# Kernel optimization log

Hardware: AMD Instinct MI355X
Metric: run time of the kernel (lower is better)

Reference implementation:

```python
import jax, jax.numpy as jnp
import numpy as np

B, H, S, D = 8, 16, 1024, 128

def setup_inputs() -> dict:
    key = jax.random.key(0)
    kq, kk, kv = jax.random.split(key, 3)
    q = jax.random.normal(kq, (B, H, S, D), dtype=jnp.float32)
    k = jax.random.normal(kk, (B, H, S, D), dtype=jnp.float32)
    v = jax.random.normal(kv, (B, H, S, D), dtype=jnp.float32)
    return {"q": q, "k": k, "v": v}

def reference(q, k, v):
    dims = q.shape[-1]
    # scores[..., j, i] = sum_k q[..., j, k] * k_[..., i, k]; note scale is 1/dims (not 1/sqrt(dims))
    scores = jnp.einsum('bhjd,bhid->bhji', q, k) / dims
    probs = jax.nn.softmax(scores, axis=-1)
    out = jnp.einsum('bhji,bhid->bhjd', probs, v)
    return out
```

## Files before the change

kernel.cpp:

```cpp
#include <hip/hip_runtime.h>

#define S_LEN 1024
#define D_DIM 128
#define KVBLK 32
#define BH_N 128

typedef __attribute__((ext_vector_type(8))) short short8;
typedef __attribute__((ext_vector_type(4))) short short4v;
typedef __attribute__((ext_vector_type(4))) float f32x4;
typedef __attribute__((ext_vector_type(16))) float f32x16;
typedef __attribute__((ext_vector_type(4))) unsigned int uint4v;

__device__ __forceinline__ unsigned short f2bf(float f) {
  union { float f; unsigned u; } x; x.f = f;
  unsigned r = x.u + 0x7fffu + ((x.u >> 16) & 1u);
  return (unsigned short)(r >> 16);
}

__device__ __forceinline__ short8 pack8(float4 a, float4 b) {
  short8 f;
  f[0] = (short)f2bf(a.x); f[1] = (short)f2bf(a.y);
  f[2] = (short)f2bf(a.z); f[3] = (short)f2bf(a.w);
  f[4] = (short)f2bf(b.x); f[5] = (short)f2bf(b.y);
  f[6] = (short)f2bf(b.z); f[7] = (short)f2bf(b.w);
  return f;
}

__device__ __forceinline__ void gload_lds16(const void* g, void* l) {
  __builtin_amdgcn_global_load_lds(
      (const __attribute__((address_space(1))) unsigned int*)g,
      (__attribute__((address_space(3))) unsigned int*)l, 16, 0, 0);
}

__global__ __launch_bounds__(256) void conv_k(const float* __restrict__ in,
                                              unsigned short* __restrict__ out,
                                              int n8) {
  int i = blockIdx.x * 256 + threadIdx.x;
  int stride = gridDim.x * 256;
  for (; i < n8; i += stride) {
    float4 a = ((const float4*)in)[i * 2];
    float4 b = ((const float4*)in)[i * 2 + 1];
    ((short8*)out)[i] = pack8(a, b);
  }
}

__global__ __launch_bounds__(256) void conv_vt(const float* __restrict__ v,
                                               unsigned short* __restrict__ vt) {
  __shared__ unsigned short tile[64][72];
  int b = blockIdx.x;
  int d0 = (b & 1) * 64;
  int s0 = ((b >> 1) & 15) * 64;
  int bh = b >> 5;
  int t = threadIdx.x;
  #pragma unroll
  for (int i = 0; i < 4; ++i) {
    int s = (t >> 4) + i * 16;
    int dl = (t & 15) * 4;
    float4 x = *(const float4*)(v + ((size_t)(bh * S_LEN) + s0 + s) * D_DIM + d0 + dl);
    tile[s][dl + 0] = f2bf(x.x); tile[s][dl + 1] = f2bf(x.y);
    tile[s][dl + 2] = f2bf(x.z); tile[s][dl + 3] = f2bf(x.w);
  }
  __syncthreads();
  #pragma unroll
  for (int i = 0; i < 2; ++i) {
    int j = i * 256 + t;
    int dl = j >> 3, sc = j & 7;
    short8 w;
    #pragma unroll
    for (int q = 0; q < 8; ++q) w[q] = (short)tile[sc * 8 + q][dl];
    *(short8*)(vt + ((size_t)(bh * D_DIM) + d0 + dl) * S_LEN + s0 + sc * 8) = w;
  }
}

__global__ __launch_bounds__(256, 4) void attn_main(
    const float* __restrict__ qg, const unsigned short* __restrict__ kbf,
    const unsigned short* __restrict__ vtbf, float* __restrict__ og) {
  __shared__ unsigned short K_lds[2][KVBLK * D_DIM];
  __shared__ unsigned short VT_lds[2][D_DIM * KVBLK];

  const int tid = threadIdx.x;
  const int lane = tid & 63;
  const int wid = tid >> 6;
  const int l31 = lane & 31;
  const int hi = lane >> 5;

  const int bid = blockIdx.x;
  const int bh = (bid & 7) | ((bid >> 6) << 3);
  const int qt = (bid >> 3) & 7;

  const size_t base = (size_t)bh * (S_LEN * D_DIM);
  const int qw = qt * 128 + wid * 32;

  short8 qf[8];
  {
    const float* qp = qg + base + (size_t)(qw + l31) * D_DIM + hi * 8;
    const float s = 0.0078125f * 1.44269504088896f;
    #pragma unroll
    for (int c = 0; c < 8; ++c) {
      float4 a = *(const float4*)(qp + c * 16);
      float4 b = *(const float4*)(qp + c * 16 + 4);
      a.x *= s; a.y *= s; a.z *= s; a.w *= s;
      b.x *= s; b.y *= s; b.z *= s; b.w *= s;
      qf[c] = pack8(a, b);
    }
  }

  float l_r = 0.f;
  f32x16 o_acc[4];
  #pragma unroll
  for (int dt = 0; dt < 4; ++dt)
    #pragma unroll
    for (int r = 0; r < 16; ++r) o_acc[dt][r] = 0.f;

  const char* kbB = (const char*)(kbf + base);
  const char* vtB = (const char*)(vtbf + (size_t)bh * (D_DIM * S_LEN));

  int koffA, koffB, voff;
  {
    int r0 = wid * 8 + (lane >> 4);
    int c = lane & 15;
    koffA = (r0 * D_DIM + ((c ^ (r0 & 7)) * 8)) * 2;
    int r1 = r0 + 4;
    koffB = (r1 * D_DIM + ((c ^ (r1 & 7)) * 8)) * 2;
    int d0 = wid * 32 + (lane >> 2);
    int c2 = lane & 3;
    voff = (d0 * S_LEN + ((c2 ^ (lane >> 4)) * 8)) * 2;
  }
  const int KRB = l31 * 256 + ((hi ^ (l31 & 7)) << 4);
  const int VRB = l31 * 64 + ((hi ^ ((l31 >> 2) & 3)) << 4);

  #define STAGE(buf, tnext)                                                    \
    {                                                                          \
      const char* ks = kbB + (tnext) * (KVBLK * D_DIM * 2);                    \
      gload_lds16(ks + koffA, &K_lds[buf][(wid * 8) * D_DIM]);                 \
      gload_lds16(ks + koffB, &K_lds[buf][(wid * 8 + 4) * D_DIM]);             \
      const char* vs = vtB + (tnext) * (KVBLK * 2);                            \
      gload_lds16(vs + voff, &VT_lds[buf][(wid * 32) * KVBLK]);                \
      gload_lds16(vs + voff + 16 * S_LEN * 2,                                  \
                  &VT_lds[buf][(wid * 32 + 16) * KVBLK]);                      \
    }

  STAGE(0, 0);
  __syncthreads();

  for (int t = 0; t < S_LEN / KVBLK; ++t) {
    const int cur = t & 1;
    if (t + 1 < S_LEN / KVBLK) STAGE(cur ^ 1, t + 1);

    const char* kl = (const char*)&K_lds[cur][0];
    const char* vl = (const char*)&VT_lds[cur][0];

    f32x16 sacc;
    #pragma unroll
    for (int r = 0; r < 16; ++r) sacc[r] = 0.f;

    __builtin_amdgcn_s_setprio(1);
    #pragma unroll
    for (int c = 0; c < 8; ++c) {
      short8 kf = *(const short8*)(kl + (KRB ^ (c << 5)));
      sacc = __builtin_amdgcn_mfma_f32_32x32x16_bf16(kf, qf[c], sacc, 0, 0, 0);
    }
    __builtin_amdgcn_s_setprio(0);

    #pragma unroll
    for (int c = 0; c < 2; ++c) {
      float p0 = exp2f(fminf(sacc[8 * c + 0], 80.f));
      float p1 = exp2f(fminf(sacc[8 * c + 1], 80.f));
      unsigned w0;
      asm("v_cvt_pk_bf16_f32 %0, %1, %2" : "=v"(w0) : "v"(p0), "v"(p1));
      float p2 = exp2f(fminf(sacc[8 * c + 2], 80.f));
      float p3 = exp2f(fminf(sacc[8 * c + 3], 80.f));
      unsigned w1;
      asm("v_cvt_pk_bf16_f32 %0, %1, %2" : "=v"(w1) : "v"(p2), "v"(p3));
      l_r += (p0 + p1) + (p2 + p3);
      float p4 = exp2f(fminf(sacc[8 * c + 4], 80.f));
      float p5 = exp2f(fminf(sacc[8 * c + 5], 80.f));
      unsigned w2;
      asm("v_cvt_pk_bf16_f32 %0, %1, %2" : "=v"(w2) : "v"(p4), "v"(p5));
      float p6 = exp2f(fminf(sacc[8 * c + 6], 80.f));
      float p7 = exp2f(fminf(sacc[8 * c + 7], 80.f));
      unsigned w3;
      asm("v_cvt_pk_bf16_f32 %0, %1, %2" : "=v"(w3) : "v"(p6), "v"(p7));
      l_r += (p4 + p5) + (p6 + p7);

      asm volatile("v_permlane32_swap_b32 %0, %1" : "+v"(w0), "+v"(w2));
      asm volatile("v_permlane32_swap_b32 %0, %1" : "+v"(w1), "+v"(w3));
      uint4v pw;
      pw[0] = w0; pw[1] = w1; pw[2] = w2; pw[3] = w3;
      short8 pa = __builtin_bit_cast(short8, pw);

      __builtin_amdgcn_s_setprio(1);
      const int vx = VRB ^ (c << 5);
      #pragma unroll
      for (int dt = 0; dt < 4; ++dt) {
        short8 vf = *(const short8*)(vl + vx + dt * 2048);
        o_acc[dt] = __builtin_amdgcn_mfma_f32_32x32x16_bf16(pa, vf, o_acc[dt], 0, 0, 0);
      }
      __builtin_amdgcn_s_setprio(0);
    }
    __syncthreads();
  }

  float lsum = l_r + __shfl_xor(l_r, 32);
  float linv = 1.0f / lsum;
  #pragma unroll
  for (int r = 0; r < 16; ++r) {
    int qr = (r & 3) + 8 * (r >> 2) + 4 * hi;
    float lv = __shfl(linv, qr, 64);
    #pragma unroll
    for (int dt = 0; dt < 4; ++dt) {
      og[base + (size_t)(qw + qr) * D_DIM + dt * 32 + l31] = o_acc[dt][r] * lv;
    }
  }
}

__global__ __launch_bounds__(256) void attn_fused(
    const float* __restrict__ qg, const float* __restrict__ kg,
    const float* __restrict__ vg, float* __restrict__ og) {
  __shared__ unsigned short K_lds[64 * D_DIM];
  __shared__ unsigned short VT_lds[D_DIM * 64];
  __shared__ unsigned short P_lds[4][16 * 64];

  const int tid = threadIdx.x;
  const int lane = tid & 63;
  const int wid = tid >> 6;
  const int l15 = lane & 15;
  const int lg = lane >> 4;

  const int bid = blockIdx.x;
  const int bh = (bid & 7) | ((bid >> 7) << 3);
  const int qt = (bid >> 3) & 15;

  const size_t base = (size_t)bh * (S_LEN * D_DIM);
  const int qw = qt * 64 + wid * 16;

  short8 qf[4];
  {
    const float* qp = qg + base + (size_t)(qw + l15) * D_DIM + lg * 8;
    #pragma unroll
    for (int c = 0; c < 4; ++c) {
      float4 a = *(const float4*)(qp + c * 32);
      float4 b = *(const float4*)(qp + c * 32 + 4);
      const float s = 0.0078125f;
      a.x *= s; a.y *= s; a.z *= s; a.w *= s;
      b.x *= s; b.y *= s; b.z *= s; b.w *= s;
      qf[c] = pack8(a, b);
    }
  }

  float m_r[4], l_r[4];
  f32x4 o_acc[8];
  #pragma unroll
  for (int r = 0; r < 4; ++r) { m_r[r] = -INFINITY; l_r[r] = 0.f; }
  #pragma unroll
  for (int dt = 0; dt < 8; ++dt) o_acc[dt] = (f32x4){0.f, 0.f, 0.f, 0.f};

  for (int kv0 = 0; kv0 < S_LEN; kv0 += 64) {
    {
      const float* kb = kg + base + (size_t)kv0 * D_DIM;
      #pragma unroll
      for (int c = tid; c < 64 * D_DIM / 8; c += 256) {
        int row = c >> 4, dc = c & 15;
        const float* p = kb + row * D_DIM + dc * 8;
        float4 a = *(const float4*)p;
        float4 b = *(const float4*)(p + 4);
        int sidx = row * 128 + ((dc * 8) ^ ((row & 7) << 3));
        *(short8*)&K_lds[sidx] = pack8(a, b);
      }
    }
    {
      const float* vb = vg + base + (size_t)kv0 * D_DIM;
      #pragma unroll
      for (int u = tid; u < (64 / 4) * (D_DIM / 4); u += 256) {
        int ib = u & 15;
        int db = u >> 4;
        const float* p = vb + (ib * 4) * D_DIM + db * 4;
        float rr[4][4];
        #pragma unroll
        for (int c = 0; c < 4; ++c) {
          float4 t = *(const float4*)(p + c * D_DIM);
          rr[c][0] = t.x; rr[c][1] = t.y; rr[c][2] = t.z; rr[c][3] = t.w;
        }
        #pragma unroll
        for (int j = 0; j < 4; ++j) {
          short4v w;
          w[0] = (short)f2bf(rr[0][j]); w[1] = (short)f2bf(rr[1][j]);
          w[2] = (short)f2bf(rr[2][j]); w[3] = (short)f2bf(rr[3][j]);
          int row = db * 4 + j;
          int sidx = row * 64 + ((ib * 4) ^ ((row & 7) << 3));
          *(short4v*)&VT_lds[sidx] = w;
        }
      }
    }
    __syncthreads();

    f32x4 sacc[4];
    #pragma unroll
    for (int tc = 0; tc < 4; ++tc) sacc[tc] = (f32x4){0.f, 0.f, 0.f, 0.f};
    #pragma unroll
    for (int tc = 0; tc < 4; ++tc) {
      int row = tc * 16 + l15;
      #pragma unroll
      for (int ck = 0; ck < 4; ++ck) {
        int sidx = row * 128 + ((ck * 32 + lg * 8) ^ ((row & 7) << 3));
        short8 kf = *(const short8*)&K_lds[sidx];
        sacc[tc] = __builtin_amdgcn_mfma_f32_16x16x32_bf16(qf[ck], kf, sacc[tc], 0, 0, 0);
      }
    }

    float alpha[4], ps[4];
    #pragma unroll
    for (int r = 0; r < 4; ++r) {
      float a = fmaxf(fmaxf(sacc[0][r], sacc[1][r]), fmaxf(sacc[2][r], sacc[3][r]));
      a = fmaxf(a, __shfl_xor(a, 1));
      a = fmaxf(a, __shfl_xor(a, 2));
      a = fmaxf(a, __shfl_xor(a, 4));
      a = fmaxf(a, __shfl_xor(a, 8));
      float mn = fmaxf(m_r[r], a);
      alpha[r] = __expf(m_r[r] - mn);
      m_r[r] = mn;
      ps[r] = 0.f;
    }
    #pragma unroll
    for (int tc = 0; tc < 4; ++tc) {
      #pragma unroll
      for (int r = 0; r < 4; ++r) {
        float p = __expf(sacc[tc][r] - m_r[r]);
        ps[r] += p;
        int prow = lg * 4 + r;
        int pcol = tc * 16 + l15;
        P_lds[wid][prow * 64 + (pcol ^ ((prow & 7) << 3))] = f2bf(p);
      }
    }
    #pragma unroll
    for (int r = 0; r < 4; ++r) {
      float s = ps[r];
      s += __shfl_xor(s, 1); s += __shfl_xor(s, 2);
      s += __shfl_xor(s, 4); s += __shfl_xor(s, 8);
      l_r[r] = l_r[r] * alpha[r] + s;
    }
    #pragma unroll
    for (int dt = 0; dt < 8; ++dt) {
      #pragma unroll
      for (int r = 0; r < 4; ++r) o_acc[dt][r] *= alpha[r];
    }

    #pragma unroll
    for (int kc = 0; kc < 2; ++kc) {
      int pidx = l15 * 64 + ((kc * 32 + lg * 8) ^ ((l15 & 7) << 3));
      short8 pf = *(const short8*)&P_lds[wid][pidx];
      #pragma unroll
      for (int dt = 0; dt < 8; ++dt) {
        int vrow = dt * 16 + l15;
        int vidx = vrow * 64 + ((kc * 32 + lg * 8) ^ ((vrow & 7) << 3));
        short8 vf = *(const short8*)&VT_lds[vidx];
        o_acc[dt] = __builtin_amdgcn_mfma_f32_16x16x32_bf16(pf, vf, o_acc[dt], 0, 0, 0);
      }
    }
    __syncthreads();
  }

  #pragma unroll
  for (int r = 0; r < 4; ++r) {
    float inv = 1.0f / l_r[r];
    float* op = og + base + (size_t)(qw + lg * 4 + r) * D_DIM + l15;
    #pragma unroll
    for (int dt = 0; dt < 8; ++dt) op[dt * 16] = o_acc[dt][r] * inv;
  }
}

extern "C" void kernel_launch(void* const* d_in, const int* in_sizes, int n_in,
                              void* d_out, int out_size, void* d_ws, size_t ws_size,
                              hipStream_t stream) {
  const float* q = (const float*)d_in[0];
  const float* k = (const float*)d_in[1];
  const float* v = (const float*)d_in[2];
  float* o = (float*)d_out;

  const size_t n_elem = (size_t)BH_N * S_LEN * D_DIM;
  const size_t need = 2 * n_elem * sizeof(unsigned short);

  if (ws_size >= need) {
    unsigned short* kbf = (unsigned short*)d_ws;
    unsigned short* vtbf = kbf + n_elem;
    conv_k<<<dim3(2048), dim3(256), 0, stream>>>(k, kbf, (int)(n_elem / 8));
    conv_vt<<<dim3(4096), dim3(256), 0, stream>>>(v, vtbf);
    attn_main<<<dim3(1024), dim3(256), 0, stream>>>(q, kbf, vtbf, o);
  } else {
    attn_fused<<<dim3(2048), dim3(256), 0, stream>>>(q, k, v, o);
  }
}
```

Measured before the change: 148.7 us.

## Process two 32-row query tiles per wave to reuse K/V fragments

Each wave now handles 64 query rows (two 32-row MFMA tiles) instead of 32, so every K and V^T fragment read from LDS feeds two MFMAs. The grid is halved to 512 blocks and launch bounds are relaxed to 2 blocks per CU to make room for the doubled accumulators. The P-packing code moves into a helper, and the two tiles' softmax work is batched before the PV MFMAs. This aims to cut LDS read traffic and global K/V loads per query, at the cost of higher register pressure, lower occupancy and only 512 blocks for a GPU with many CUs.

Measured after the change: 152.9 us. 2.8% more time.

```diff
diff --git a/kernel.cpp b/kernel.cpp
--- a/kernel.cpp
+++ b/kernel.cpp
@@ -30,6 +30,32 @@
   __builtin_amdgcn_global_load_lds(
       (const __attribute__((address_space(1))) unsigned int*)g,
       (__attribute__((address_space(3))) unsigned int*)l, 16, 0, 0);
+}
+
+__device__ __forceinline__ short8 packP(const f32x16 sacc, const int c, float& l_r) {
+  float p0 = exp2f(fminf(sacc[8 * c + 0], 80.f));
+  float p1 = exp2f(fminf(sacc[8 * c + 1], 80.f));
+  unsigned w0;
+  asm("v_cvt_pk_bf16_f32 %0, %1, %2" : "=v"(w0) : "v"(p0), "v"(p1));
+  float p2 = exp2f(fminf(sacc[8 * c + 2], 80.f));
+  float p3 = exp2f(fminf(sacc[8 * c + 3], 80.f));
+  unsigned w1;
+  asm("v_cvt_pk_bf16_f32 %0, %1, %2" : "=v"(w1) : "v"(p2), "v"(p3));
+  l_r += (p0 + p1) + (p2 + p3);
+  float p4 = exp2f(fminf(sacc[8 * c + 4], 80.f));
+  float p5 = exp2f(fminf(sacc[8 * c + 5], 80.f));
+  unsigned w2;
+  asm("v_cvt_pk_bf16_f32 %0, %1, %2" : "=v"(w2) : "v"(p4), "v"(p5));
+  float p6 = exp2f(fminf(sacc[8 * c + 6], 80.f));
+  float p7 = exp2f(fminf(sacc[8 * c + 7], 80.f));
+  unsigned w3;
+  asm("v_cvt_pk_bf16_f32 %0, %1, %2" : "=v"(w3) : "v"(p6), "v"(p7));
+  l_r += (p4 + p5) + (p6 + p7);
+  asm volatile("v_permlane32_swap_b32 %0, %1" : "+v"(w0), "+v"(w2));
+  asm volatile("v_permlane32_swap_b32 %0, %1" : "+v"(w1), "+v"(w3));
+  uint4v pw;
+  pw[0] = w0; pw[1] = w1; pw[2] = w2; pw[3] = w3;
+  return __builtin_bit_cast(short8, pw);
 }
 
 __global__ __launch_bounds__(256) void conv_k(const float* __restrict__ in,
@@ -72,7 +98,7 @@
   }
 }
 
-__global__ __launch_bounds__(256, 4) void attn_main(
+__global__ __launch_bounds__(256, 2) void attn_main(
     const float* __restrict__ qg, const unsigned short* __restrict__ kbf,
     const unsigned short* __restrict__ vtbf, float* __restrict__ og) {
   __shared__ unsigned short K_lds[2][KVBLK * D_DIM];
@@ -85,32 +111,38 @@
   const int hi = lane >> 5;
 
   const int bid = blockIdx.x;
-  const int bh = (bid & 7) | ((bid >> 6) << 3);
-  const int qt = (bid >> 3) & 7;
+  const int bh = (bid & 7) | ((bid >> 5) << 3);
+  const int qt = (bid >> 3) & 3;
 
   const size_t base = (size_t)bh * (S_LEN * D_DIM);
-  const int qw = qt * 128 + wid * 32;
-
-  short8 qf[8];
+  const int qw = qt * 256 + wid * 64;
+
+  short8 qfA[8], qfB[8];
   {
-    const float* qp = qg + base + (size_t)(qw + l31) * D_DIM + hi * 8;
     const float s = 0.0078125f * 1.44269504088896f;
+    const float* qpA = qg + base + (size_t)(qw + l31) * D_DIM + hi * 8;
+    const float* qpB = qpA + 32 * D_DIM;
     #pragma unroll
     for (int c = 0; c < 8; ++c) {
-      float4 a = *(const float4*)(qp + c * 16);
-      float4 b = *(const float4*)(qp + c * 16 + 4);
+      float4 a = *(const float4*)(qpA + c * 16);
+      float4 b = *(const float4*)(qpA + c * 16 + 4);
       a.x *= s; a.y *= s; a.z *= s; a.w *= s;
       b.x *= s; b.y *= s; b.z *= s; b.w *= s;
-      qf[c] = pack8(a, b);
-    }
-  }
-
-  float l_r = 0.f;
-  f32x16 o_acc[4];
+      qfA[c] = pack8(a, b);
+      float4 e = *(const float4*)(qpB + c * 16);
+      float4 f = *(const float4*)(qpB + c * 16 + 4);
+      e.x *= s; e.y *= s; e.z *= s; e.w *= s;
+      f.x *= s; f.y *= s; f.z *= s; f.w *= s;
+      qfB[c] = pack8(e, f);
+    }
+  }
+
+  float lA = 0.f, lB = 0.f;
+  f32x16 oA[4], oB[4];
   #pragma unroll
   for (int dt = 0; dt < 4; ++dt)
     #pragma unroll
-    for (int r = 0; r < 16; ++r) o_acc[dt][r] = 0.f;
+    for (int r = 0; r < 16; ++r) { oA[dt][r] = 0.f; oB[dt][r] = 0.f; }
 
   const char* kbB = (const char*)(kbf + base);
   const char* vtB = (const char*)(vtbf + (size_t)bh * (D_DIM * S_LEN));
@@ -150,66 +182,58 @@
     const char* kl = (const char*)&K_lds[cur][0];
     const char* vl = (const char*)&VT_lds[cur][0];
 
-    f32x16 sacc;
-    #pragma unroll
-    for (int r = 0; r < 16; ++r) sacc[r] = 0.f;
+    f32x16 sA, sB;
+    #pragma unroll
+    for (int r = 0; r < 16; ++r) { sA[r] = 0.f; sB[r] = 0.f; }
 
     __builtin_amdgcn_s_setprio(1);
     #pragma unroll
     for (int c = 0; c < 8; ++c) {
       short8 kf = *(const short8*)(kl + (KRB ^ (c << 5)));
-      sacc = __builtin_amdgcn_mfma_f32_32x32x16_bf16(kf, qf[c], sacc, 0, 0, 0);
+      sA = __builtin_amdgcn_mfma_f32_32x32x16_bf16(kf, qfA[c], sA, 0, 0, 0);
+      sB = __builtin_amdgcn_mfma_f32_32x32x16_bf16(kf, qfB[c], sB, 0, 0, 0);
     }
     __builtin_amdgcn_s_setprio(0);
 
-    #pragma unroll
-    for (int c = 0; c < 2; ++c) {
-      float p0 = exp2f(fminf(sacc[8 * c + 0], 80.f));
-      float p1 = exp2f(fminf(sacc[8 * c + 1], 80.f));
-      unsigned w0;
-      asm("v_cvt_pk_bf16_f32 %0, %1, %2" : "=v"(w0) : "v"(p0), "v"(p1));
-      float p2 = exp2f(fminf(sacc[8 * c + 2], 80.f));
-      float p3 = exp2f(fminf(sacc[8 * c + 3], 80.f));
-      unsigned w1;
-      asm("v_cvt_pk_bf16_f32 %0, %1, %2" : "=v"(w1) : "v"(p2), "v"(p3));
-      l_r += (p0 + p1) + (p2 + p3);
-      float p4 = exp2f(fminf(sacc[8 * c + 4], 80.f));
-      float p5 = exp2f(fminf(sacc[8 * c + 5], 80.f));
-      unsigned w2;
-      asm("v_cvt_pk_bf16_f32 %0, %1, %2" : "=v"(w2) : "v"(p4), "v"(p5));
-      float p6 = exp2f(fminf(sacc[8 * c + 6], 80.f));
-      float p7 = exp2f(fminf(sacc[8 * c + 7], 80.f));
-      unsigned w3;
-      asm("v_cvt_pk_bf16_f32 %0, %1, %2" : "=v"(w3) : "v"(p6), "v"(p7));
-      l_r += (p4 + p5) + (p6 + p7);
-
-      asm volatile("v_permlane32_swap_b32 %0, %1" : "+v"(w0), "+v"(w2));
-      asm volatile("v_permlane32_swap_b32 %0, %1" : "+v"(w1), "+v"(w3));
-      uint4v pw;
-      pw[0] = w0; pw[1] = w1; pw[2] = w2; pw[3] = w3;
-      short8 pa = __builtin_bit_cast(short8, pw);
-
-      __builtin_amdgcn_s_setprio(1);
-      const int vx = VRB ^ (c << 5);
+    short8 paA0 = packP(sA, 0, lA);
+    short8 paA1 = packP(sA, 1, lA);
+    short8 paB0 = packP(sB, 0, lB);
+    short8 paB1 = packP(sB, 1, lB);
+
+    __builtin_amdgcn_s_setprio(1);
+    {
+      const int vx0 = VRB;
       #pragma unroll
       for (int dt = 0; dt < 4; ++dt) {
-        short8 vf = *(const short8*)(vl + vx + dt * 2048);
-        o_acc[dt] = __builtin_amdgcn_mfma_f32_32x32x16_bf16(pa, vf, o_acc[dt], 0, 0, 0);
-      }
-      __builtin_amdgcn_s_setprio(0);
-    }
+        short8 vf = *(const short8*)(vl + vx0 + dt * 2048);
+        oA[dt] = __builtin_amdgcn_mfma_f32_32x32x16_bf16(paA0, vf, oA[dt], 0, 0, 0);
+        oB[dt] = __builtin_amdgcn_mfma_f32_32x32x16_bf16(paB0, vf, oB[dt], 0, 0, 0);
+      }
+      const int vx1 = VRB ^ 32;
+      #pragma unroll
+      for (int dt = 0; dt < 4; ++dt) {
+        short8 vf = *(const short8*)(vl + vx1 + dt * 2048);
+        oA[dt] = __builtin_amdgcn_mfma_f32_32x32x16_bf16(paA1, vf, oA[dt], 0, 0, 0);
+        oB[dt] = __builtin_amdgcn_mfma_f32_32x32x16_bf16(paB1, vf, oB[dt], 0, 0, 0);
+      }
+    }
+    __builtin_amdgcn_s_setprio(0);
     __syncthreads();
   }
 
-  float lsum = l_r + __shfl_xor(l_r, 32);
-  float linv = 1.0f / lsum;
+  float lsA = lA + __shfl_xor(lA, 32);
+  float liA = 1.0f / lsA;
+  float lsB = lB + __shfl_xor(lB, 32);
+  float liB = 1.0f / lsB;
   #pragma unroll
   for (int r = 0; r < 16; ++r) {
     int qr = (r & 3) + 8 * (r >> 2) + 4 * hi;
-    float lv = __shfl(linv, qr, 64);
+    float lvA = __shfl(liA, qr, 64);
+    float lvB = __shfl(liB, qr, 64);
     #pragma unroll
     for (int dt = 0; dt < 4; ++dt) {
-      og[base + (size_t)(qw + qr) * D_DIM + dt * 32 + l31] = o_acc[dt][r] * lv;
+      og[base + (size_t)(qw + qr) * D_DIM + dt * 32 + l31] = oA[dt][r] * lvA;
+      og[base + (size_t)(qw + 32 + qr) * D_DIM + dt * 32 + l31] = oB[dt][r] * lvB;
     }
   }
 }
@@ -385,7 +409,7 @@
     unsigned short* vtbf = kbf + n_elem;
     conv_k<<<dim3(2048), dim3(256), 0, stream>>>(k, kbf, (int)(n_elem / 8));
     conv_vt<<<dim3(4096), dim3(256), 0, stream>>>(v, vtbf);
-    attn_main<<<dim3(1024), dim3(256), 0, stream>>>(q, kbf, vtbf, o);
+    attn_main<<<dim3(512), dim3(256), 0, stream>>>(q, kbf, vtbf, o);
   } else {
     attn_fused<<<dim3(2048), dim3(256), 0, stream>>>(q, k, v, o);
   }
```

## Software-pipeline attention loop with triple-buffered LDS and QK of next tile

Applied to the files above, without the earlier changes.

Switches the K/V LDS staging from double to triple buffering, prefetching two tiles ahead. It also restructures the loop so the QK^T MFMAs for the next tile are issued while softmax packing and PV MFMAs run on the current tile. The goal is to hide exp/convert latency and global-load latency behind matrix work. In exchange it raises LDS use and register pressure, so launch bounds drop to 3 blocks per CU, and it removes the s_setprio hints.

Result: faster. 139.3 us (-6.3%).

```diff
diff --git a/kernel.cpp b/kernel.cpp
--- a/kernel.cpp
+++ b/kernel.cpp
@@ -3,6 +3,7 @@
 #define S_LEN 1024
 #define D_DIM 128
 #define KVBLK 32
+#define NT (S_LEN / KVBLK)
 #define BH_N 128
 
 typedef __attribute__((ext_vector_type(8))) short short8;
@@ -30,6 +31,32 @@
   __builtin_amdgcn_global_load_lds(
       (const __attribute__((address_space(1))) unsigned int*)g,
       (__attribute__((address_space(3))) unsigned int*)l, 16, 0, 0);
+}
+
+__device__ __forceinline__ short8 packP(const f32x16 sacc, const int c, float& l_r) {
+  float p0 = exp2f(fminf(sacc[8 * c + 0], 80.f));
+  float p1 = exp2f(fminf(sacc[8 * c + 1], 80.f));
+  unsigned w0;
+  asm("v_cvt_pk_bf16_f32 %0, %1, %2" : "=v"(w0) : "v"(p0), "v"(p1));
+  float p2 = exp2f(fminf(sacc[8 * c + 2], 80.f));
+  float p3 = exp2f(fminf(sacc[8 * c + 3], 80.f));
+  unsigned w1;
+  asm("v_cvt_pk_bf16_f32 %0, %1, %2" : "=v"(w1) : "v"(p2), "v"(p3));
+  l_r += (p0 + p1) + (p2 + p3);
+  float p4 = exp2f(fminf(sacc[8 * c + 4], 80.f));
+  float p5 = exp2f(fminf(sacc[8 * c + 5], 80.f));
+  unsigned w2;
+  asm("v_cvt_pk_bf16_f32 %0, %1, %2" : "=v"(w2) : "v"(p4), "v"(p5));
+  float p6 = exp2f(fminf(sacc[8 * c + 6], 80.f));
+  float p7 = exp2f(fminf(sacc[8 * c + 7], 80.f));
+  unsigned w3;
+  asm("v_cvt_pk_bf16_f32 %0, %1, %2" : "=v"(w3) : "v"(p6), "v"(p7));
+  l_r += (p4 + p5) + (p6 + p7);
+  asm volatile("v_permlane32_swap_b32 %0, %1" : "+v"(w0), "+v"(w2));
+  asm volatile("v_permlane32_swap_b32 %0, %1" : "+v"(w1), "+v"(w3));
+  uint4v pw;
+  pw[0] = w0; pw[1] = w1; pw[2] = w2; pw[3] = w3;
+  return __builtin_bit_cast(short8, pw);
 }
 
 __global__ __launch_bounds__(256) void conv_k(const float* __restrict__ in,
@@ -72,11 +99,11 @@
   }
 }
 
-__global__ __launch_bounds__(256, 4) void attn_main(
+__global__ __launch_bounds__(256, 3) void attn_main(
     const float* __restrict__ qg, const unsigned short* __restrict__ kbf,
     const unsigned short* __restrict__ vtbf, float* __restrict__ og) {
-  __shared__ unsigned short K_lds[2][KVBLK * D_DIM];
-  __shared__ unsigned short VT_lds[2][D_DIM * KVBLK];
+  __shared__ unsigned short K_lds[3][KVBLK * D_DIM];
+  __shared__ unsigned short VT_lds[3][D_DIM * KVBLK];
 
   const int tid = threadIdx.x;
   const int lane = tid & 63;
@@ -129,76 +156,78 @@
   const int KRB = l31 * 256 + ((hi ^ (l31 & 7)) << 4);
   const int VRB = l31 * 64 + ((hi ^ ((l31 >> 2) & 3)) << 4);
 
-  #define STAGE(buf, tnext)                                                    \
+  #define STAGE(slot, tnext)                                                   \
     {                                                                          \
       const char* ks = kbB + (tnext) * (KVBLK * D_DIM * 2);                    \
-      gload_lds16(ks + koffA, &K_lds[buf][(wid * 8) * D_DIM]);                 \
-      gload_lds16(ks + koffB, &K_lds[buf][(wid * 8 + 4) * D_DIM]);             \
+      gload_lds16(ks + koffA, &K_lds[slot][(wid * 8) * D_DIM]);                \
+      gload_lds16(ks + koffB, &K_lds[slot][(wid * 8 + 4) * D_DIM]);            \
       const char* vs = vtB + (tnext) * (KVBLK * 2);                            \
-      gload_lds16(vs + voff, &VT_lds[buf][(wid * 32) * KVBLK]);                \
+      gload_lds16(vs + voff, &VT_lds[slot][(wid * 32) * KVBLK]);               \
       gload_lds16(vs + voff + 16 * S_LEN * 2,                                  \
-                  &VT_lds[buf][(wid * 32 + 16) * KVBLK]);                      \
+                  &VT_lds[slot][(wid * 32 + 16) * KVBLK]);                     \
+    }
+
+  #define QKT(slot, dst)                                                       \
+    {                                                                          \
+      const char* kl = (const char*)&K_lds[slot][0];                           \
+      f32x16 s_;                                                               \
+      _Pragma("unroll")                                                        \
+      for (int r = 0; r < 16; ++r) s_[r] = 0.f;                                \
+      _Pragma("unroll")                                                        \
+      for (int c = 0; c < 8; ++c) {                                            \
+        short8 kf = *(const short8*)(kl + (KRB ^ (c << 5)));                   \
+        s_ = __builtin_amdgcn_mfma_f32_32x32x16_bf16(kf, qf[c], s_, 0, 0, 0);  \
+      }                                                                        \
+      dst = s_;                                                                \
+    }
+
+  #define PV(slot, pa0, pa1)                                                   \
+    {                                                                          \
+      const char* vl = (const char*)&VT_lds[slot][0];                          \
+      _Pragma("unroll")                                                        \
+      for (int dt = 0; dt < 4; ++dt) {                                         \
+        short8 vf = *(const short8*)(vl + (VRB) + dt * 2048);                  \
+        o_acc[dt] = __builtin_amdgcn_mfma_f32_32x32x16_bf16(pa0, vf, o_acc[dt], 0, 0, 0); \
+      }                                                                        \
+      _Pragma("unroll")                                                        \
+      for (int dt = 0; dt < 4; ++dt) {                                         \
+        short8 vf = *(const short8*)(vl + (VRB ^ 32) + dt * 2048);             \
+        o_acc[dt] = __builtin_amdgcn_mfma_f32_32x32x16_bf16(pa1, vf, o_acc[dt], 0, 0, 0); \
+      }                                                                        \
     }
 
   STAGE(0, 0);
+  STAGE(1, 1);
   __syncthreads();
 
-  for (int t = 0; t < S_LEN / KVBLK; ++t) {
-    const int cur = t & 1;
-    if (t + 1 < S_LEN / KVBLK) STAGE(cur ^ 1, t + 1);
-
-    const char* kl = (const char*)&K_lds[cur][0];
-    const char* vl = (const char*)&VT_lds[cur][0];
-
-    f32x16 sacc;
-    #pragma unroll
-    for (int r = 0; r < 16; ++r) sacc[r] = 0.f;
-
-    __builtin_amdgcn_s_setprio(1);
-    #pragma unroll
-    for (int c = 0; c < 8; ++c) {
-      short8 kf = *(const short8*)(kl + (KRB ^ (c << 5)));
-      sacc = __builtin_amdgcn_mfma_f32_32x32x16_bf16(kf, qf[c], sacc, 0, 0, 0);
-    }
-    __builtin_amdgcn_s_setprio(0);
-
-    #pragma unroll
-    for (int c = 0; c < 2; ++c) {
-      float p0 = exp2f(fminf(sacc[8 * c + 0], 80.f));
-      float p1 = exp2f(fminf(sacc[8 * c + 1], 80.f));
-      unsigned w0;
-      asm("v_cvt_pk_bf16_f32 %0, %1, %2" : "=v"(w0) : "v"(p0), "v"(p1));
-      float p2 = exp2f(fminf(sacc[8 * c + 2], 80.f));
-      float p3 = exp2f(fminf(sacc[8 * c + 3], 80.f));
-      unsigned w1;
-      asm("v_cvt_pk_bf16_f32 %0, %1, %2" : "=v"(w1) : "v"(p2), "v"(p3));
-      l_r += (p0 + p1) + (p2 + p3);
-      float p4 = exp2f(fminf(sacc[8 * c + 4], 80.f));
-      float p5 = exp2f(fminf(sacc[8 * c + 5], 80.f));
-      unsigned w2;
-      asm("v_cvt_pk_bf16_f32 %0, %1, %2" : "=v"(w2) : "v"(p4), "v"(p5));
-      float p6 = exp2f(fminf(sacc[8 * c + 6], 80.f));
-      float p7 = exp2f(fminf(sacc[8 * c + 7], 80.f));
-      unsigned w3;
-      asm("v_cvt_pk_bf16_f32 %0, %1, %2" : "=v"(w3) : "v"(p6), "v"(p7));
-      l_r += (p4 + p5) + (p6 + p7);
-
-      asm volatile("v_permlane32_swap_b32 %0, %1" : "+v"(w0), "+v"(w2));
-      asm volatile("v_permlane32_swap_b32 %0, %1" : "+v"(w1), "+v"(w3));
-      uint4v pw;
-      pw[0] = w0; pw[1] = w1; pw[2] = w2; pw[3] = w3;
-      short8 pa = __builtin_bit_cast(short8, pw);
-
-      __builtin_amdgcn_s_setprio(1);
-      const int vx = VRB ^ (c << 5);
-      #pragma unroll
-      for (int dt = 0; dt < 4; ++dt) {
-        short8 vf = *(const short8*)(vl + vx + dt * 2048);
-        o_acc[dt] = __builtin_amdgcn_mfma_f32_32x32x16_bf16(pa, vf, o_acc[dt], 0, 0, 0);
-      }
-      __builtin_amdgcn_s_setprio(0);
-    }
+  f32x16 sacc;
+  QKT(0, sacc);
+
+  int sl = 0;
+  for (int t = 0; t < NT - 2; ++t) {
+    int slN = sl + 1; if (slN == 3) slN = 0;
+    int slNN = slN + 1; if (slNN == 3) slNN = 0;
+    STAGE(slNN, t + 2);
+    short8 pa0 = packP(sacc, 0, l_r);
+    short8 pa1 = packP(sacc, 1, l_r);
+    QKT(slN, sacc);
+    PV(sl, pa0, pa1);
     __syncthreads();
+    sl = slN;
+  }
+  {
+    int slN = sl + 1; if (slN == 3) slN = 0;
+    short8 pa0 = packP(sacc, 0, l_r);
+    short8 pa1 = packP(sacc, 1, l_r);
+    QKT(slN, sacc);
+    PV(sl, pa0, pa1);
+    __syncthreads();
+    sl = slN;
+  }
+  {
+    short8 pa0 = packP(sacc, 0, l_r);
+    short8 pa1 = packP(sacc, 1, l_r);
+    PV(sl, pa0, pa1);
   }
 
   float lsum = l_r + __shfl_xor(l_r, 32);
```
